# Kernel optimization log

Hardware: AMD Instinct MI355X
Metric: run time of the kernel (lower is better)

Reference implementation:

```python
import jax, jax.numpy as jnp
import numpy as np

B, S, P, C = 128, 672, 168, 500  # batch, seq_len, pred_len, channels

def setup_inputs() -> dict:
    key = jax.random.key(0)
    k1, k2, k3 = jax.random.split(key, 3)
    x = jax.random.normal(k1, (B, S, C), dtype=jnp.float32)
    # per-channel Linear(seq_len -> pred_len): W[c] is [pred_len, seq_len], b[c] is [pred_len]
    W = jax.random.normal(k2, (C, P, S), dtype=jnp.float32) * (1.0 / np.sqrt(S))
    b = jax.random.normal(k3, (C, P), dtype=jnp.float32) * (1.0 / np.sqrt(S))
    return {"x": x, "W": W, "b": b}

def reference(x, W, b):
    # NLinear: subtract last time step, per-channel linear over time, add back
    seq_last = x[:, -1:, :]                     # [B, 1, C]
    xc = x - seq_last                           # [B, S, C]
    # batched over channels: out[b,p,c] = sum_s xc[b,s,c] * W[c,p,s] + b[c,p]
    out = jnp.einsum('bsc,cps->bpc', xc, W) + b.T[None, :, :]
    return out + seq_last
```

## Files before the change

kernel.cpp:

```cpp
#include <hip/hip_runtime.h>


typedef __attribute__((ext_vector_type(8))) short short8;
typedef __attribute__((ext_vector_type(4))) float floatx4;

namespace {
constexpr int Bn = 128, Sn = 672, Pn = 168, Cn = 500;
constexpr int XQ_CSTRIDE = Bn * Sn;
constexpr int TC = 64, TS = 96, TROW = TS + 12;
constexpr int BC   = 2;
constexpr int BPAD = 96;
constexpr int NSCH = Sn / 32;
constexpr int A_ELE = BC * Bn * 32;
constexpr int W_ELE = BC * BPAD * 32;
constexpr int NWORK = 500;
}

__device__ __forceinline__ unsigned short f2bf(float f) {
  unsigned int u = __builtin_bit_cast(unsigned int, f);
  u += 0x7fffu + ((u >> 16) & 1u);
  return (unsigned short)(u >> 16);
}

__global__ __launch_bounds__(256)
void xpose_kernel(const float* __restrict__ x, unsigned short* __restrict__ xq) {
  __shared__ unsigned short T[TC][TROW];
  const int b  = blockIdx.x;
  const int s0 = blockIdx.y * TS;
  const int c0 = blockIdx.z * TC;
  const int t  = threadIdx.x;

  #pragma unroll
  for (int i = 0; i < 6; ++i) {
    const int idx = t + i * 256;
    const int sr  = idx >> 4;
    const int cq  = (idx & 15) * 4;
    int c = c0 + cq;
    if (c > Cn - 4) c = Cn - 4;
    const int rel = c - c0;
    const float4 xv = *(const float4*)&x[(size_t)(b * Sn + s0 + sr) * Cn + c];
    const float4 xl = *(const float4*)&x[(size_t)(b * Sn + (Sn - 1)) * Cn + c];
    T[rel + 0][sr] = f2bf(xv.x - xl.x);
    T[rel + 1][sr] = f2bf(xv.y - xl.y);
    T[rel + 2][sr] = f2bf(xv.z - xl.z);
    T[rel + 3][sr] = f2bf(xv.w - xl.w);
  }
  __syncthreads();
  #pragma unroll
  for (int i = 0; i < 6; ++i) {
    const int idx = t + i * 256;
    const int cr  = idx / 24;
    const int sq  = (idx % 24) * 4;
    const int c   = c0 + cr;
    if (c >= Cn) continue;
    const ushort4 v = *(const ushort4*)&T[cr][sq];
    *(ushort4*)&xq[(size_t)c * XQ_CSTRIDE + b * Sn + s0 + sq] = v;
  }
}

__global__ __launch_bounds__(512, 4)
void gemm_kernel(const unsigned short* __restrict__ xq, const float* __restrict__ W,
                 const float* __restrict__ bias, const float* __restrict__ x,
                 float* __restrict__ out) {
  __shared__ unsigned short As[2][A_ELE];
  __shared__ unsigned short Ws[2][W_ELE];

  const int wid = (blockIdx.x & 7) * 64 + (blockIdx.x >> 3);
  if (wid >= NWORK) return;
  const int pt = wid & 1;
  const int c0 = (wid >> 1) * BC;
  const int p_base = pt * BPAD;

  const int tid  = threadIdx.x;
  const int lane = tid & 63;
  const int wave = tid >> 6;
  const int r16  = lane & 15;
  const int kg   = lane >> 4;
  const int bw   = wave & 3;
  const int pw   = wave >> 2;

  int ag[2], aw[2];
  #pragma unroll
  for (int r = 0; r < 2; ++r) {
    const int idx = r * 512 + tid;
    const int g  = idx & 3;
    const int b  = (idx >> 2) & 127;
    const int cc = idx >> 9;
    ag[r] = (c0 + cc) * XQ_CSTRIDE + b * Sn + g * 8;
    aw[r] = (cc * Bn + b) * 32 + ((g ^ ((b >> 1) & 3)) * 8);
  }
  int wg[3], ww[3];
  #pragma unroll
  for (int r = 0; r < 3; ++r) {
    const int idx  = r * 512 + tid;
    const int q    = idx & 7;
    const int row  = idx >> 3;
    const int cc   = row / BPAD;
    const int prow = row - cc * BPAD;
    int p = p_base + prow;
    if (p >= Pn) p = Pn - 1;
    wg[r] = ((c0 + cc) * Pn + p) * Sn + q * 4;
    const int g = q >> 1, half = q & 1;
    ww[r] = (cc * BPAD + prow) * 32 + ((g ^ ((prow >> 1) & 3)) * 8) + half * 4;
  }

  int ard[2][2];
  int wrd[2][3];
  #pragma unroll
  for (int cc = 0; cc < 2; ++cc) {
    #pragma unroll
    for (int fb = 0; fb < 2; ++fb) {
      const int row = bw * 32 + fb * 16 + r16;
      ard[cc][fb] = (cc * Bn + row) * 32 + ((kg ^ ((row >> 1) & 3)) * 8);
    }
    #pragma unroll
    for (int fp = 0; fp < 3; ++fp) {
      const int prow = pw * 48 + fp * 16 + r16;
      wrd[cc][fp] = (cc * BPAD + prow) * 32 + ((kg ^ ((prow >> 1) & 3)) * 8);
    }
  }

  floatx4 acc[2][3][2];
  #pragma unroll
  for (int fb = 0; fb < 2; ++fb)
    #pragma unroll
    for (int fp = 0; fp < 3; ++fp)
      #pragma unroll
      for (int cc = 0; cc < 2; ++cc)
        acc[fb][fp][cc] = (floatx4){0.f, 0.f, 0.f, 0.f};

  short8 rA0a, rA0b; float4 rW0a, rW0b, rW0c;
  short8 rA1a, rA1b; float4 rW1a, rW1b, rW1c;

  auto load0 = [&](int sch) {
    const int so = sch * 32;
    rA0a = *(const short8*)(xq + ag[0] + so);
    rA0b = *(const short8*)(xq + ag[1] + so);
    rW0a = *(const float4*)(W + wg[0] + so);
    rW0b = *(const float4*)(W + wg[1] + so);
    rW0c = *(const float4*)(W + wg[2] + so);
  };
  auto load1 = [&](int sch) {
    const int so = sch * 32;
    rA1a = *(const short8*)(xq + ag[0] + so);
    rA1b = *(const short8*)(xq + ag[1] + so);
    rW1a = *(const float4*)(W + wg[0] + so);
    rW1b = *(const float4*)(W + wg[1] + so);
    rW1c = *(const float4*)(W + wg[2] + so);
  };
  auto store0 = [&](int buf) {
    *(short8*)&As[buf][aw[0]] = rA0a;
    *(short8*)&As[buf][aw[1]] = rA0b;
    ushort4 u;
    u.x = f2bf(rW0a.x); u.y = f2bf(rW0a.y); u.z = f2bf(rW0a.z); u.w = f2bf(rW0a.w);
    *(ushort4*)&Ws[buf][ww[0]] = u;
    u.x = f2bf(rW0b.x); u.y = f2bf(rW0b.y); u.z = f2bf(rW0b.z); u.w = f2bf(rW0b.w);
    *(ushort4*)&Ws[buf][ww[1]] = u;
    u.x = f2bf(rW0c.x); u.y = f2bf(rW0c.y); u.z = f2bf(rW0c.z); u.w = f2bf(rW0c.w);
    *(ushort4*)&Ws[buf][ww[2]] = u;
  };
  auto store1 = [&](int buf) {
    *(short8*)&As[buf][aw[0]] = rA1a;
    *(short8*)&As[buf][aw[1]] = rA1b;
    ushort4 u;
    u.x = f2bf(rW1a.x); u.y = f2bf(rW1a.y); u.z = f2bf(rW1a.z); u.w = f2bf(rW1a.w);
    *(ushort4*)&Ws[buf][ww[0]] = u;
    u.x = f2bf(rW1b.x); u.y = f2bf(rW1b.y); u.z = f2bf(rW1b.z); u.w = f2bf(rW1b.w);
    *(ushort4*)&Ws[buf][ww[1]] = u;
    u.x = f2bf(rW1c.x); u.y = f2bf(rW1c.y); u.z = f2bf(rW1c.z); u.w = f2bf(rW1c.w);
    *(ushort4*)&Ws[buf][ww[2]] = u;
  };
  auto compute = [&](int buf) {
    #pragma unroll
    for (int cc = 0; cc < 2; ++cc) {
      short8 af[2], wf[3];
      #pragma unroll
      for (int fb = 0; fb < 2; ++fb) af[fb] = *(const short8*)&As[buf][ard[cc][fb]];
      #pragma unroll
      for (int fp = 0; fp < 3; ++fp) wf[fp] = *(const short8*)&Ws[buf][wrd[cc][fp]];
      #pragma unroll
      for (int fb = 0; fb < 2; ++fb)
        #pragma unroll
        for (int fp = 0; fp < 3; ++fp)
          acc[fb][fp][cc] =
              __builtin_amdgcn_mfma_f32_16x16x32_bf16(af[fb], wf[fp], acc[fb][fp][cc], 0, 0, 0);
    }
  };

  load0(0);
  load1(1);
  store0(0);
  __syncthreads();

  #pragma unroll 1
  for (int k = 0; k < NSCH - 1; k += 2) {
    if (k + 2 < NSCH) load0(k + 2);
    compute(0);
    store1(1);
    __syncthreads();
    if (k + 3 < NSCH) load1(k + 3);
    compute(1);
    if (k + 2 < NSCH) store0(0);
    __syncthreads();
  }
  compute(0);

  float2 xl[2][4];
  #pragma unroll
  for (int fb = 0; fb < 2; ++fb)
    #pragma unroll
    for (int r = 0; r < 4; ++r) {
      const int b = bw * 32 + fb * 16 + kg * 4 + r;
      xl[fb][r] = *(const float2*)&x[(size_t)(b * Sn + Sn - 1) * Cn + c0];
    }
  #pragma unroll
  for (int fp = 0; fp < 3; ++fp) {
    const int p = p_base + pw * 48 + fp * 16 + r16;
    if (p >= Pn) continue;
    const float b0 = bias[(size_t)(c0 + 0) * Pn + p];
    const float b1 = bias[(size_t)(c0 + 1) * Pn + p];
    #pragma unroll
    for (int fb = 0; fb < 2; ++fb)
      #pragma unroll
      for (int r = 0; r < 4; ++r) {
        const int b = bw * 32 + fb * 16 + kg * 4 + r;
        float2 st;
        st.x = acc[fb][fp][0][r] + b0 + xl[fb][r].x;
        st.y = acc[fb][fp][1][r] + b1 + xl[fb][r].y;
        *(float2*)&out[(size_t)(b * Pn + p) * Cn + c0] = st;
      }
  }
}

extern "C" void kernel_launch(void* const* d_in, const int* in_sizes, int n_in,
                              void* d_out, int out_size, void* d_ws, size_t ws_size,
                              hipStream_t stream) {
  (void)in_sizes; (void)n_in; (void)out_size; (void)ws_size;
  const float* x  = (const float*)d_in[0];
  const float* W  = (const float*)d_in[1];
  const float* bv = (const float*)d_in[2];
  float* out = (float*)d_out;
  unsigned short* xq = (unsigned short*)d_ws;

  hipLaunchKernelGGL(xpose_kernel, dim3(Bn, Sn / TS, (Cn + TC - 1) / TC), dim3(256), 0, stream,
                     x, xq);
  hipLaunchKernelGGL(gemm_kernel, dim3(512), dim3(512), 0, stream,
                     xq, W, bv, x, out);
}
```

Before: 171.4 us.

## Load activation tiles straight into LDS and pre-swizzle them in the transpose

The activation (A) tile now goes from global memory straight into shared memory with global_load_lds, skipping the register staging and the LDS store instructions. The LDS bank-conflict swizzle that used to be applied on the LDS write is now applied when the transpose kernel writes xq, so the direct LDS copy can use a plain per-wave linear layout. The main-loop barriers become a custom s_waitcnt vmcnt(3)/s_barrier sequence, so the newest weight loads can still be in flight while the A data is guaranteed to have landed. This relies on vmcnt ordering and on a matching layout between the two kernels, which makes it more fragile.

```diff
diff --git a/kernel.cpp b/kernel.cpp
--- a/kernel.cpp
+++ b/kernel.cpp
@@ -22,6 +22,12 @@
   return (unsigned short)(u >> 16);
 }
 
+__device__ __forceinline__ void gload16(const unsigned short* g, unsigned short* l) {
+  __builtin_amdgcn_global_load_lds(
+      (const __attribute__((address_space(1))) unsigned int*)g,
+      (__attribute__((address_space(3))) unsigned int*)l, 16, 0, 0);
+}
+
 __global__ __launch_bounds__(256)
 void xpose_kernel(const float* __restrict__ x, unsigned short* __restrict__ xq) {
   __shared__ unsigned short T[TC][TROW];
@@ -29,6 +35,7 @@
   const int s0 = blockIdx.y * TS;
   const int c0 = blockIdx.z * TC;
   const int t  = threadIdx.x;
+  const int sw = (b >> 1) & 3;
 
   #pragma unroll
   for (int i = 0; i < 6; ++i) {
@@ -54,9 +61,13 @@
     const int c   = c0 + cr;
     if (c >= Cn) continue;
     const ushort4 v = *(const ushort4*)&T[cr][sq];
-    *(ushort4*)&xq[(size_t)c * XQ_CSTRIDE + b * Sn + s0 + sq] = v;
-  }
-}
+    const int o   = (sq >> 3) & 3;
+    const int sqw = (sq & ~31) | (((o ^ sw) & 3) << 3) | (sq & 7);
+    *(ushort4*)&xq[(size_t)c * XQ_CSTRIDE + b * Sn + s0 + sqw] = v;
+  }
+}
+
+#define WAIT_BAR(N) asm volatile("s_waitcnt vmcnt(" #N ") lgkmcnt(0)\n\ts_barrier" ::: "memory")
 
 __global__ __launch_bounds__(512, 4)
 void gemm_kernel(const unsigned short* __restrict__ xq, const float* __restrict__ W,
@@ -79,7 +90,7 @@
   const int bw   = wave & 3;
   const int pw   = wave >> 2;
 
-  int ag[2], aw[2];
+  int ag[2];
   #pragma unroll
   for (int r = 0; r < 2; ++r) {
     const int idx = r * 512 + tid;
@@ -87,8 +98,10 @@
     const int b  = (idx >> 2) & 127;
     const int cc = idx >> 9;
     ag[r] = (c0 + cc) * XQ_CSTRIDE + b * Sn + g * 8;
-    aw[r] = (cc * Bn + b) * 32 + ((g ^ ((b >> 1) & 3)) * 8);
-  }
+  }
+  const int ldsA0 = (wave * 64 + (tid & 63) - (tid & 63)) * 0 + wave * 512;
+  const int ldsA1 = 4096 + wave * 512;
+
   int wg[3], ww[3];
   #pragma unroll
   for (int r = 0; r < 3; ++r) {
@@ -104,8 +117,7 @@
     ww[r] = (cc * BPAD + prow) * 32 + ((g ^ ((prow >> 1) & 3)) * 8) + half * 4;
   }
 
-  int ard[2][2];
-  int wrd[2][3];
+  int ard[2][2], wrd[2][3];
   #pragma unroll
   for (int cc = 0; cc < 2; ++cc) {
     #pragma unroll
@@ -129,45 +141,42 @@
       for (int cc = 0; cc < 2; ++cc)
         acc[fb][fp][cc] = (floatx4){0.f, 0.f, 0.f, 0.f};
 
-  short8 rA0a, rA0b; float4 rW0a, rW0b, rW0c;
-  short8 rA1a, rA1b; float4 rW1a, rW1b, rW1c;
-
-  auto load0 = [&](int sch) {
+  float4 s0a, s0b, s0c;
+  float4 s1a, s1b, s1c;
+
+  auto issueA = [&](int sch, int buf) {
     const int so = sch * 32;
-    rA0a = *(const short8*)(xq + ag[0] + so);
-    rA0b = *(const short8*)(xq + ag[1] + so);
-    rW0a = *(const float4*)(W + wg[0] + so);
-    rW0b = *(const float4*)(W + wg[1] + so);
-    rW0c = *(const float4*)(W + wg[2] + so);
-  };
-  auto load1 = [&](int sch) {
+    gload16(xq + ag[0] + so, &As[buf][ldsA0]);
+    gload16(xq + ag[1] + so, &As[buf][ldsA1]);
+  };
+  auto issueW0 = [&](int sch) {
     const int so = sch * 32;
-    rA1a = *(const short8*)(xq + ag[0] + so);
-    rA1b = *(const short8*)(xq + ag[1] + so);
-    rW1a = *(const float4*)(W + wg[0] + so);
-    rW1b = *(const float4*)(W + wg[1] + so);
-    rW1c = *(const float4*)(W + wg[2] + so);
-  };
-  auto store0 = [&](int buf) {
-    *(short8*)&As[buf][aw[0]] = rA0a;
-    *(short8*)&As[buf][aw[1]] = rA0b;
+    s0a = *(const float4*)(W + wg[0] + so);
+    s0b = *(const float4*)(W + wg[1] + so);
+    s0c = *(const float4*)(W + wg[2] + so);
+  };
+  auto issueW1 = [&](int sch) {
+    const int so = sch * 32;
+    s1a = *(const float4*)(W + wg[0] + so);
+    s1b = *(const float4*)(W + wg[1] + so);
+    s1c = *(const float4*)(W + wg[2] + so);
+  };
+  auto storeW0 = [&](int buf) {
     ushort4 u;
-    u.x = f2bf(rW0a.x); u.y = f2bf(rW0a.y); u.z = f2bf(rW0a.z); u.w = f2bf(rW0a.w);
+    u.x = f2bf(s0a.x); u.y = f2bf(s0a.y); u.z = f2bf(s0a.z); u.w = f2bf(s0a.w);
     *(ushort4*)&Ws[buf][ww[0]] = u;
-    u.x = f2bf(rW0b.x); u.y = f2bf(rW0b.y); u.z = f2bf(rW0b.z); u.w = f2bf(rW0b.w);
+    u.x = f2bf(s0b.x); u.y = f2bf(s0b.y); u.z = f2bf(s0b.z); u.w = f2bf(s0b.w);
     *(ushort4*)&Ws[buf][ww[1]] = u;
-    u.x = f2bf(rW0c.x); u.y = f2bf(rW0c.y); u.z = f2bf(rW0c.z); u.w = f2bf(rW0c.w);
+    u.x = f2bf(s0c.x); u.y = f2bf(s0c.y); u.z = f2bf(s0c.z); u.w = f2bf(s0c.w);
     *(ushort4*)&Ws[buf][ww[2]] = u;
   };
-  auto store1 = [&](int buf) {
-    *(short8*)&As[buf][aw[0]] = rA1a;
-    *(short8*)&As[buf][aw[1]] = rA1b;
+  auto storeW1 = [&](int buf) {
     ushort4 u;
-    u.x = f2bf(rW1a.x); u.y = f2bf(rW1a.y); u.z = f2bf(rW1a.z); u.w = f2bf(rW1a.w);
+    u.x = f2bf(s1a.x); u.y = f2bf(s1a.y); u.z = f2bf(s1a.z); u.w = f2bf(s1a.w);
     *(ushort4*)&Ws[buf][ww[0]] = u;
-    u.x = f2bf(rW1b.x); u.y = f2bf(rW1b.y); u.z = f2bf(rW1b.z); u.w = f2bf(rW1b.w);
+    u.x = f2bf(s1b.x); u.y = f2bf(s1b.y); u.z = f2bf(s1b.z); u.w = f2bf(s1b.w);
     *(ushort4*)&Ws[buf][ww[1]] = u;
-    u.x = f2bf(rW1c.x); u.y = f2bf(rW1c.y); u.z = f2bf(rW1c.z); u.w = f2bf(rW1c.w);
+    u.x = f2bf(s1c.x); u.y = f2bf(s1c.y); u.z = f2bf(s1c.z); u.w = f2bf(s1c.w);
     *(ushort4*)&Ws[buf][ww[2]] = u;
   };
   auto compute = [&](int buf) {
@@ -187,21 +196,30 @@
     }
   };
 
-  load0(0);
-  load1(1);
-  store0(0);
-  __syncthreads();
+  issueA(0, 0);
+  issueW0(0);
+  issueW1(1);
+  storeW0(0);
+  WAIT_BAR(3);
 
   #pragma unroll 1
-  for (int k = 0; k < NSCH - 1; k += 2) {
-    if (k + 2 < NSCH) load0(k + 2);
+  for (int jj = 0; jj < NSCH - 1; jj += 2) {
+    issueA(jj + 1, 1);
+    issueW0(jj + 2);
     compute(0);
-    store1(1);
-    __syncthreads();
-    if (k + 3 < NSCH) load1(k + 3);
-    compute(1);
-    if (k + 2 < NSCH) store0(0);
-    __syncthreads();
+    storeW1(1);
+    WAIT_BAR(3);
+    issueA(jj + 2, 0);
+    if (jj < NSCH - 3) {
+      issueW1(jj + 3);
+      compute(1);
+      storeW0(0);
+      WAIT_BAR(3);
+    } else {
+      compute(1);
+      storeW0(0);
+      WAIT_BAR(0);
+    }
   }
   compute(0);
 
```

New measurement: 260.3 us. 1.52x slower.
